# Kernel tuning notes

Hardware: AMD Instinct MI355X
Metric: run time of the kernel (lower is better)

## Reference

```python
import jax, jax.numpy as jnp
import numpy as np

B, S, D, H = 2, 2048, 1024, 16
DH = D // H          # 64, even -> RoPE valid
ROPE_BASE = 10000.0
LN_EPS = 1e-5


def _rope_cache(seq_len, head_dim, dtype):
    half = head_dim // 2
    inv_freq = 1.0 / (ROPE_BASE ** (jnp.arange(half, dtype=jnp.float32) / half))
    t = jnp.arange(seq_len, dtype=jnp.float32)
    freqs = t[:, None] * inv_freq[None, :]            # [S, half]
    emb = jnp.concatenate([freqs, freqs], axis=-1)    # [S, DH]
    return jnp.cos(emb).astype(dtype)[None, None], jnp.sin(emb).astype(dtype)[None, None]


def _rotate_every_two(x):
    x_even = x[..., ::2]
    x_odd = x[..., 1::2]
    return jnp.stack([-x_odd, x_even], axis=-1).reshape(x.shape)


def setup_inputs() -> dict:
    key = jax.random.key(0)
    ks = jax.random.split(key, 4)
    w = lambda k, shape: (jax.random.normal(k, shape, jnp.float32) * 0.02)
    return {
        "x_qk": jax.random.normal(ks[0], (B, S, D), jnp.float32),
        "x_v": jax.random.normal(ks[1], (B, S, D), jnp.float32),
        "W_qk": w(ks[2], (D, 2 * D)),
        "b_qk": jnp.zeros((2 * D,), jnp.float32),
        "W_v": w(ks[3], (D, D)),
        "b_v": jnp.zeros((D,), jnp.float32),
        "ln_gamma": jnp.ones((D,), jnp.float32),
        "ln_beta": jnp.zeros((D,), jnp.float32),
    }


def reference(x_qk, x_v, W_qk, b_qk, W_v, b_v, ln_gamma, ln_beta):
    b, s, d = x_qk.shape
    # fused QK projection -> [B,S,2,H,DH]
    qk = (x_qk @ W_qk + b_qk).reshape(b, s, 2, H, DH)
    q = jnp.transpose(qk[:, :, 0], (0, 2, 1, 3))  # [B,H,S,DH]
    k = jnp.transpose(qk[:, :, 1], (0, 2, 1, 3))
    v = jnp.transpose((x_v @ W_v + b_v).reshape(b, s, H, DH), (0, 2, 1, 3))

    cos, sin = _rope_cache(s, DH, q.dtype)
    q = q * cos + _rotate_every_two(q) * sin
    k = k * cos + _rotate_every_two(k) * sin

    scale = 1.0 / jnp.sqrt(jnp.asarray(DH, q.dtype))
    scores = jnp.einsum("bhqd,bhkd->bhqk", q, k) * scale
    probs = jax.nn.softmax(scores, axis=-1)
    attn = jnp.einsum("bhqk,bhkd->bhqd", probs, v)      # [B,H,S,DH]
    attn = jnp.transpose(attn, (0, 2, 1, 3)).reshape(b, s, d)

    mu = jnp.mean(attn, axis=-1, keepdims=True)
    var = jnp.var(attn, axis=-1, keepdims=True)
    out = (attn - mu) * jax.lax.rsqrt(var + LN_EPS) * ln_gamma + ln_beta
    return out
```

## Files before the change

kernel.cpp:

```cpp
#include <hip/hip_runtime.h>
#include <hip/hip_bf16.h>

#define Bn 2
#define Sn 2048
#define Dn 1024
#define Hn 16
#define DHn 64
#define Kd 1024
#define Mn (Bn * Sn)
#define LN10K 9.210340371976184f

typedef __attribute__((ext_vector_type(8))) short bf16x8;
typedef __attribute__((ext_vector_type(4))) float f32x4;
typedef __attribute__((ext_vector_type(16))) float f32x16;

static __device__ __forceinline__ ushort f2bf(float f) {
    uint u = __float_as_uint(f);
    u += 0x7fff + ((u >> 16) & 1);
    return (ushort)(u >> 16);
}
static __device__ __forceinline__ uint cvtpk(float a, float b) {
    uint r;
    asm("v_cvt_pk_bf16_f32 %0, %1, %2" : "=v"(r) : "v"(a), "v"(b));
    return r;
}
static __device__ __forceinline__ void plswap(uint& a, uint& b) {
    asm volatile("v_permlane32_swap_b32 %0, %1" : "+v"(a), "+v"(b));
}

#define MFMA16(a, b, c) __builtin_amdgcn_mfma_f32_16x16x32_bf16((a), (b), (c), 0, 0, 0)
#define MFMA32(a, b, c) __builtin_amdgcn_mfma_f32_32x32x16_bf16((a), (b), (c), 0, 0, 0)

static __device__ __forceinline__ void gload16(const ushort* g, ushort* l) {
    __builtin_amdgcn_global_load_lds(
        (const __attribute__((address_space(1))) void*)g,
        (__attribute__((address_space(3))) void*)l, 16, 0, 0);
}

static __device__ __forceinline__ int swz(int row, int col16) {
    return row * 128 + (((col16) * 16) ^ ((row & 7) << 4));
}

__global__ __launch_bounds__(256) void rope_tab(float* __restrict__ ct,
                                                float* __restrict__ st)
{
    const int idx = blockIdx.x * 256 + threadIdx.x;
    const int s = idx >> 5, fe = idx & 31;
    const float f = expf(-LN10K * (float)fe / 32.0f);
    const float a = (float)s * f;
    ct[idx] = cosf(a);
    st[idx] = sinf(a);
}

__global__ __launch_bounds__(256) void cvt_bf16(const float* __restrict__ in,
                                                ushort* __restrict__ out)
{
    const size_t i = ((size_t)blockIdx.x * 256 + threadIdx.x) * 8;
    const float4 a = *(const float4*)(in + i);
    const float4 b = *(const float4*)(in + i + 4);
    ushort4 lo = make_ushort4(f2bf(a.x), f2bf(a.y), f2bf(a.z), f2bf(a.w));
    ushort4 hi = make_ushort4(f2bf(b.x), f2bf(b.y), f2bf(b.z), f2bf(b.w));
    *(ushort4*)(out + i) = lo;
    *(ushort4*)(out + i + 4) = hi;
}

__global__ __launch_bounds__(256) void transpose_bf16(
    const float* __restrict__ in, ushort* __restrict__ out, int R, int C)
{
    __shared__ ushort t[32][33];
    const int n0 = blockIdx.x * 32, k0 = blockIdx.y * 32;
    const int x = threadIdx.x, y = threadIdx.y;
#pragma unroll
    for (int i = 0; i < 4; ++i)
        t[y + 8 * i][x] = f2bf(in[(size_t)(k0 + y + 8 * i) * C + n0 + x]);
    __syncthreads();
#pragma unroll
    for (int i = 0; i < 4; ++i)
        out[(size_t)(n0 + y + 8 * i) * R + k0 + x] = t[x][y + 8 * i];
}

template <int MODE>
__global__ __launch_bounds__(256) void gemm_mfma(
    const ushort* __restrict__ A, const ushort* __restrict__ Bt,
    const float* __restrict__ bias, const float* __restrict__ ctab,
    const float* __restrict__ stab, ushort* __restrict__ o0,
    ushort* __restrict__ o1)
{
    __shared__ ushort Asm[128 * 64];
    __shared__ ushort Bsm[128 * 64];

    const int tid = threadIdx.x;
    const int lane = tid & 63, w = tid >> 6;
    const int g = lane >> 4, c = lane & 15;
    const int mbase = blockIdx.y * 128;
    const int nbase = blockIdx.x * 128;
    const int wm = (w >> 1) * 64, wn = (w & 1) * 64;

    f32x4 acc[4][4];
#pragma unroll
    for (int mf = 0; mf < 4; ++mf)
#pragma unroll
        for (int nf = 0; nf < 4; ++nf)
            acc[mf][nf] = (f32x4){0.f, 0.f, 0.f, 0.f};

    const int sbase = w * 64 + lane;

    for (int k0 = 0; k0 < Kd; k0 += 64) {
#pragma unroll
        for (int j = 0; j < 4; ++j) {
            const int i = j * 256 + sbase;
            const int row = i >> 3, c16 = i & 7;
            const int kc = (c16 ^ (row & 7)) * 8;
            gload16(A + (size_t)(mbase + row) * Kd + k0 + kc,
                    &Asm[(size_t)(j * 256 + w * 64) * 8]);
            gload16(Bt + (size_t)(nbase + row) * Kd + k0 + kc,
                    &Bsm[(size_t)(j * 256 + w * 64) * 8]);
        }
        __syncthreads();

#pragma unroll
        for (int ks = 0; ks < 2; ++ks) {
            bf16x8 af[4], bfr[4];
#pragma unroll
            for (int mf = 0; mf < 4; ++mf) {
                const int row = wm + mf * 16 + c;
                af[mf] = *(const bf16x8*)((const char*)Asm + swz(row, ks * 4 + g));
            }
#pragma unroll
            for (int nf = 0; nf < 4; ++nf) {
                const int row = wn + nf * 16 + c;
                bfr[nf] = *(const bf16x8*)((const char*)Bsm + swz(row, ks * 4 + g));
            }
#pragma unroll
            for (int mf = 0; mf < 4; ++mf)
#pragma unroll
                for (int nf = 0; nf < 4; ++nf)
                    acc[mf][nf] = MFMA16(af[mf], bfr[nf], acc[mf][nf]);
        }
        __syncthreads();
    }

#pragma unroll
    for (int nf = 0; nf < 4; ++nf) {
        const int col = nbase + wn + nf * 16 + c;
        const float bs = bias[col];
        if (MODE == 0) {
            const int dh = col & 63, h = (col >> 6) & 15, isK = col >> 10;
            ushort* dst = isK ? o1 : o0;
            const float sc = isK ? 1.0f : 0.18033688011112042f;
            const float* cr = ctab + (dh & 31);
            const float* sr = stab + (dh & 31);
#pragma unroll
            for (int mf = 0; mf < 4; ++mf) {
#pragma unroll
                for (int r = 0; r < 4; ++r) {
                    const int row = mbase + wm + mf * 16 + g * 4 + r;
                    const int s = row & 2047, b = row >> 11;
                    const float v = acc[mf][nf][r] + bs;
                    const float p = __shfl_xor(v, 1);
                    const float cs = cr[s * 32], sn = sr[s * 32];
                    const float ov = (c & 1) ? v * cs + p * sn
                                             : v * cs - p * sn;
                    dst[(((size_t)(b * Hn + h)) * Sn + s) * DHn + dh] =
                        f2bf(ov * sc);
                }
            }
        } else {
            const int h = col >> 6, dh = col & 63;
#pragma unroll
            for (int mf = 0; mf < 4; ++mf) {
#pragma unroll
                for (int r = 0; r < 4; ++r) {
                    const int row = mbase + wm + mf * 16 + g * 4 + r;
                    const int s = row & 2047, b = row >> 11;
                    const float v = acc[mf][nf][r] + bs;
                    o0[(((size_t)(b * Hn + h)) * DHn + dh) * Sn + s] = f2bf(v);
                }
            }
        }
    }
}

__global__ __launch_bounds__(256) void attn_mfma(
    const ushort* __restrict__ Qg, const ushort* __restrict__ Kg,
    const ushort* __restrict__ Vtg, float* __restrict__ Aw)
{
    __shared__ char Kt[3][8192];
    __shared__ char Vt[3][8192];

    const int tid = threadIdx.x;
    const int lane = tid & 63, w = tid >> 6;
    const int r31 = lane & 31, hi = lane >> 5;
    const int bh = blockIdx.y;
    const int b = bh >> 4, h = bh & 15;
    const int q0 = blockIdx.x * 128 + w * 32;

    const ushort* qp = Qg + ((size_t)bh * Sn + q0 + r31) * DHn + hi * 8;
    bf16x8 qf[4];
#pragma unroll
    for (int kt = 0; kt < 4; ++kt)
        qf[kt] = *(const bf16x8*)(qp + kt * 16);

    const ushort* Kb = Kg + (size_t)bh * Sn * DHn;
    const ushort* Vb = Vtg + (size_t)bh * DHn * Sn;

    auto stage = [&](int buf, int kb) {
#pragma unroll
        for (int j = 0; j < 2; ++j) {
            const int i = j * 256 + w * 64 + lane;
            const int row = i >> 3, c16 = i & 7;
            const int kc = (c16 ^ (row & 7)) * 8;
            gload16(Kb + (size_t)(kb + row) * DHn + kc,
                    (ushort*)&Kt[buf][(j * 256 + w * 64) * 16]);
            gload16(Vb + (size_t)row * Sn + kb + kc,
                    (ushort*)&Vt[buf][(j * 256 + w * 64) * 16]);
        }
    };

    stage(0, 0);
    stage(1, 64);

    f32x16 acc0, acc1;
#pragma unroll
    for (int i = 0; i < 16; ++i) { acc0[i] = 0.f; acc1[i] = 0.f; }
    float m = -1e30f, lp = 0.f;

    const int NT = Sn / 64;
    for (int t = 0; t < NT; ++t) {
        const int cur = t % 3;

        if (t < NT - 1) {
            asm volatile("s_waitcnt vmcnt(4)" ::: "memory");
        } else {
            asm volatile("s_waitcnt vmcnt(0)" ::: "memory");
        }
        __builtin_amdgcn_sched_barrier(0);
        __builtin_amdgcn_s_barrier();
        __builtin_amdgcn_sched_barrier(0);

        f32x16 C0, C1;
#pragma unroll
        for (int i = 0; i < 16; ++i) { C0[i] = 0.f; C1[i] = 0.f; }
        __builtin_amdgcn_s_setprio(1);
#pragma unroll
        for (int kt = 0; kt < 4; ++kt) {
            const bf16x8 ka = *(const bf16x8*)&Kt[cur][swz(r31, kt * 2 + hi)];
            C0 = MFMA32(ka, qf[kt], C0);
        }
#pragma unroll
        for (int kt = 0; kt < 4; ++kt) {
            const bf16x8 ka = *(const bf16x8*)&Kt[cur][swz(32 + r31, kt * 2 + hi)];
            C1 = MFMA32(ka, qf[kt], C1);
        }
        __builtin_amdgcn_s_setprio(0);

        float mx[8];
#pragma unroll
        for (int i = 0; i < 8; ++i)
            mx[i] = fmaxf(fmaxf(C0[i], C0[i + 8]), fmaxf(C1[i], C1[i + 8]));
        mx[0] = fmaxf(mx[0], mx[4]); mx[1] = fmaxf(mx[1], mx[5]);
        mx[2] = fmaxf(mx[2], mx[6]); mx[3] = fmaxf(mx[3], mx[7]);
        float pmax = fmaxf(fmaxf(mx[0], mx[1]), fmaxf(mx[2], mx[3]));
        pmax = fmaxf(pmax, __shfl_xor(pmax, 32));

        if (__any(pmax > m + 11.5f)) {
            const float mn = fmaxf(m, pmax);
            const float a = exp2f(m - mn);
            m = mn;
            lp *= a;
#pragma unroll
            for (int reg = 0; reg < 16; ++reg) {
                const int qr = (reg & 3) + 8 * (reg >> 2) + 4 * hi;
                const float ar = __shfl(a, qr);
                acc0[reg] *= ar;
                acc1[reg] *= ar;
            }
        }

        bf16x8 paf[4];
#pragma unroll
        for (int tile = 0; tile < 2; ++tile) {
            const f32x16& C = tile ? C1 : C0;
            float e[16];
#pragma unroll
            for (int i = 0; i < 16; ++i) e[i] = exp2f(C[i] - m);
            float s = 0.f;
#pragma unroll
            for (int i = 0; i < 16; ++i) s += e[i];
            lp += s;
            uint p01 = cvtpk(e[0], e[1]),  p23 = cvtpk(e[2], e[3]);
            uint p45 = cvtpk(e[4], e[5]),  p67 = cvtpk(e[6], e[7]);
            uint p89 = cvtpk(e[8], e[9]),  pab = cvtpk(e[10], e[11]);
            uint pcd = cvtpk(e[12], e[13]), pef = cvtpk(e[14], e[15]);
            plswap(p01, p45); plswap(p23, p67);
            plswap(p89, pcd); plswap(pab, pef);
            uint4 f0 = {p01, p23, p45, p67};
            uint4 f1 = {p89, pab, pcd, pef};
            paf[tile * 2 + 0] = *(const bf16x8*)&f0;
            paf[tile * 2 + 1] = *(const bf16x8*)&f1;
        }

        __builtin_amdgcn_s_setprio(1);
#pragma unroll
        for (int kf = 0; kf < 4; ++kf) {
            const bf16x8 v0 = *(const bf16x8*)&Vt[cur][swz(r31, kf * 2 + hi)];
            acc0 = MFMA32(paf[kf], v0, acc0);
        }
#pragma unroll
        for (int kf = 0; kf < 4; ++kf) {
            const bf16x8 v1 = *(const bf16x8*)&Vt[cur][swz(32 + r31, kf * 2 + hi)];
            acc1 = MFMA32(paf[kf], v1, acc1);
        }
        __builtin_amdgcn_s_setprio(0);

        __builtin_amdgcn_sched_barrier(0);
        if (t + 2 < NT) stage((t + 2) % 3, (t + 2) * 64);
    }

    const float lv = lp + __shfl_xor(lp, 32);
    const float inv = 1.0f / lv;
#pragma unroll
    for (int reg = 0; reg < 16; ++reg) {
        const int qr = (reg & 3) + 8 * (reg >> 2) + 4 * hi;
        const float ir = __shfl(inv, qr);
        const int qs = q0 + qr;
        float* dst = &Aw[((size_t)b * Sn + qs) * Dn + h * DHn + r31];
        dst[0]  = acc0[reg] * ir;
        dst[32] = acc1[reg] * ir;
    }
}

__global__ __launch_bounds__(256) void ln_kernel(
    const float* __restrict__ Aw, const float* __restrict__ gamma,
    const float* __restrict__ beta, float* __restrict__ out)
{
    const int row = blockIdx.x;
    const int tid = threadIdx.x;
    const int d0 = tid * 4;
    const float4 x = *(const float4*)&Aw[(size_t)row * Dn + d0];
    float sum = x.x + x.y + x.z + x.w;
    float sq = x.x * x.x + x.y * x.y + x.z * x.z + x.w * x.w;
    for (int off = 32; off; off >>= 1) {
        sum += __shfl_xor(sum, off);
        sq += __shfl_xor(sq, off);
    }
    __shared__ float red[8];
    const int lane = tid & 63, wave = tid >> 6;
    if (lane == 0) { red[wave] = sum; red[wave + 4] = sq; }
    __syncthreads();
    if (tid == 0) {
        red[0] = red[0] + red[1] + red[2] + red[3];
        red[4] = red[4] + red[5] + red[6] + red[7];
    }
    __syncthreads();
    sum = red[0]; sq = red[4];
    const float mu = sum * (1.0f / Dn);
    const float var = sq * (1.0f / Dn) - mu * mu;
    const float rs = rsqrtf(var + 1e-5f);

    const float4 gv = *(const float4*)&gamma[d0];
    const float4 bv = *(const float4*)&beta[d0];
    float4 ov;
    ov.x = (x.x - mu) * rs * gv.x + bv.x;
    ov.y = (x.y - mu) * rs * gv.y + bv.y;
    ov.z = (x.z - mu) * rs * gv.z + bv.z;
    ov.w = (x.w - mu) * rs * gv.w + bv.w;
    *(float4*)&out[(size_t)row * Dn + d0] = ov;
}

extern "C" void kernel_launch(void* const* d_in, const int* in_sizes, int n_in,
                              void* d_out, int out_size, void* d_ws, size_t ws_size,
                              hipStream_t stream)
{
    const float* x_qk = (const float*)d_in[0];
    const float* x_v  = (const float*)d_in[1];
    const float* W_qk = (const float*)d_in[2];
    const float* b_qk = (const float*)d_in[3];
    const float* W_v  = (const float*)d_in[4];
    const float* b_v  = (const float*)d_in[5];
    const float* g    = (const float*)d_in[6];
    const float* be   = (const float*)d_in[7];

    char* ws = (char*)d_ws;
    ushort* Qw    = (ushort*)(ws);
    ushort* Kw    = (ushort*)(ws + (8u  << 20));
    ushort* Vtw   = (ushort*)(ws + (16u << 20));
    float*  Aw    = (float*) (ws + (24u << 20));
    ushort* xqkB  = (ushort*)(ws + (40u << 20));
    ushort* xvB   = (ushort*)(ws + (48u << 20));
    ushort* WqkT  = (ushort*)(ws + (56u << 20));
    ushort* WvT   = (ushort*)(ws + (60u << 20));
    float*  ctab  = (float*) (ws + (62u << 20));
    float*  stab  = (float*) (ws + (62u << 20) + (256u << 10));

    rope_tab<<<256, 256, 0, stream>>>(ctab, stab);
    cvt_bf16<<<2048, 256, 0, stream>>>(x_qk, xqkB);
    cvt_bf16<<<2048, 256, 0, stream>>>(x_v, xvB);
    transpose_bf16<<<dim3(64, 32), dim3(32, 8), 0, stream>>>(W_qk, WqkT, Kd, 2048);
    transpose_bf16<<<dim3(32, 32), dim3(32, 8), 0, stream>>>(W_v, WvT, Kd, 1024);

    gemm_mfma<0><<<dim3(16, 32), 256, 0, stream>>>(
        xqkB, WqkT, b_qk, ctab, stab, Qw, Kw);
    gemm_mfma<1><<<dim3(8, 32), 256, 0, stream>>>(
        xvB, WvT, b_v, ctab, stab, Vtw, nullptr);

    attn_mfma<<<dim3(16, 32), 256, 0, stream>>>(Qw, Kw, Vtw, Aw);
    ln_kernel<<<Bn * Sn, 256, 0, stream>>>(Aw, g, be, (float*)d_out);
}
```

Baseline: 168.3 us.

## Merge preprocessing kernels into one launch and fuse QK and V projection GEMMs

Combines rope table generation, input bf16 conversion and weight transposes into a single block-indexed prep kernel. The QK and V projection GEMMs are merged into one launch whose grid covers both, choosing inputs and epilogue per block. This removes several kernel launches and inter-kernel gaps and improves wave occupancy across the GPU, at the cost of a runtime branch in the epilogue and divergent block roles.

```diff
diff --git a/kernel.cpp b/kernel.cpp
--- a/kernel.cpp
+++ b/kernel.cpp
@@ -41,59 +41,74 @@
     return row * 128 + (((col16) * 16) ^ ((row & 7) << 4));
 }
 
-__global__ __launch_bounds__(256) void rope_tab(float* __restrict__ ct,
-                                                float* __restrict__ st)
+__global__ __launch_bounds__(256) void prep(
+    const float* __restrict__ x_qk, const float* __restrict__ x_v,
+    const float* __restrict__ W_qk, const float* __restrict__ W_v,
+    ushort* __restrict__ xqkB, ushort* __restrict__ xvB,
+    ushort* __restrict__ WqkT, ushort* __restrict__ WvT,
+    float* __restrict__ ct, float* __restrict__ st)
 {
-    const int idx = blockIdx.x * 256 + threadIdx.x;
-    const int s = idx >> 5, fe = idx & 31;
-    const float f = expf(-LN10K * (float)fe / 32.0f);
-    const float a = (float)s * f;
-    ct[idx] = cosf(a);
-    st[idx] = sinf(a);
-}
-
-__global__ __launch_bounds__(256) void cvt_bf16(const float* __restrict__ in,
-                                                ushort* __restrict__ out)
-{
-    const size_t i = ((size_t)blockIdx.x * 256 + threadIdx.x) * 8;
-    const float4 a = *(const float4*)(in + i);
-    const float4 b = *(const float4*)(in + i + 4);
-    ushort4 lo = make_ushort4(f2bf(a.x), f2bf(a.y), f2bf(a.z), f2bf(a.w));
-    ushort4 hi = make_ushort4(f2bf(b.x), f2bf(b.y), f2bf(b.z), f2bf(b.w));
-    *(ushort4*)(out + i) = lo;
-    *(ushort4*)(out + i + 4) = hi;
-}
-
-__global__ __launch_bounds__(256) void transpose_bf16(
-    const float* __restrict__ in, ushort* __restrict__ out, int R, int C)
-{
-    __shared__ ushort t[32][33];
-    const int n0 = blockIdx.x * 32, k0 = blockIdx.y * 32;
-    const int x = threadIdx.x, y = threadIdx.y;
-#pragma unroll
-    for (int i = 0; i < 4; ++i)
-        t[y + 8 * i][x] = f2bf(in[(size_t)(k0 + y + 8 * i) * C + n0 + x]);
-    __syncthreads();
-#pragma unroll
-    for (int i = 0; i < 4; ++i)
-        out[(size_t)(n0 + y + 8 * i) * R + k0 + x] = t[x][y + 8 * i];
-}
-
-template <int MODE>
-__global__ __launch_bounds__(256) void gemm_mfma(
-    const ushort* __restrict__ A, const ushort* __restrict__ Bt,
-    const float* __restrict__ bias, const float* __restrict__ ctab,
-    const float* __restrict__ stab, ushort* __restrict__ o0,
-    ushort* __restrict__ o1)
+    __shared__ ushort tle[32][33];
+    const int blk = blockIdx.x;
+    const int tid = threadIdx.x;
+
+    if (blk < 4096) {
+        const float* in = (blk < 2048) ? x_qk : x_v;
+        ushort* out = (blk < 2048) ? xqkB : xvB;
+        const int lb = (blk < 2048) ? blk : blk - 2048;
+        const size_t i = ((size_t)lb * 256 + tid) * 8;
+        const float4 a = *(const float4*)(in + i);
+        const float4 b = *(const float4*)(in + i + 4);
+        *(ushort4*)(out + i) =
+            make_ushort4(f2bf(a.x), f2bf(a.y), f2bf(a.z), f2bf(a.w));
+        *(ushort4*)(out + i + 4) =
+            make_ushort4(f2bf(b.x), f2bf(b.y), f2bf(b.z), f2bf(b.w));
+    } else if (blk < 7168) {
+        const bool isQK = blk < 6144;
+        const int t = isQK ? blk - 4096 : blk - 6144;
+        const int C = isQK ? 2048 : 1024;
+        const float* in = isQK ? W_qk : W_v;
+        ushort* out = isQK ? WqkT : WvT;
+        const int n0 = (isQK ? (t & 63) : (t & 31)) * 32;
+        const int k0 = (isQK ? (t >> 6) : (t >> 5)) * 32;
+        const int x = tid & 31, y = tid >> 5;
+#pragma unroll
+        for (int i = 0; i < 4; ++i)
+            tle[y + 8 * i][x] = f2bf(in[(size_t)(k0 + y + 8 * i) * C + n0 + x]);
+        __syncthreads();
+#pragma unroll
+        for (int i = 0; i < 4; ++i)
+            out[(size_t)(n0 + y + 8 * i) * Kd + k0 + x] = tle[x][y + 8 * i];
+    } else {
+        const int idx = (blk - 7168) * 256 + tid;
+        const int s = idx >> 5, fe = idx & 31;
+        const float f = expf(-LN10K * (float)fe / 32.0f);
+        const float a = (float)s * f;
+        ct[idx] = cosf(a);
+        st[idx] = sinf(a);
+    }
+}
+
+__global__ __launch_bounds__(256) void gemm_fused_all(
+    const ushort* __restrict__ xqkB, const ushort* __restrict__ xvB,
+    const ushort* __restrict__ WqkT, const ushort* __restrict__ WvT,
+    const float* __restrict__ b_qk, const float* __restrict__ b_v,
+    const float* __restrict__ ctab, const float* __restrict__ stab,
+    ushort* __restrict__ Qw, ushort* __restrict__ Kw, ushort* __restrict__ Vtw)
 {
     __shared__ ushort Asm[128 * 64];
     __shared__ ushort Bsm[128 * 64];
 
+    const bool isQK = blockIdx.x < 16;
+    const ushort* A  = isQK ? xqkB : xvB;
+    const ushort* Bt = isQK ? WqkT : WvT;
+    const float* bias = isQK ? b_qk : b_v;
+    const int nbase = (isQK ? blockIdx.x : blockIdx.x - 16) * 128;
+    const int mbase = blockIdx.y * 128;
+
     const int tid = threadIdx.x;
     const int lane = tid & 63, w = tid >> 6;
     const int g = lane >> 4, c = lane & 15;
-    const int mbase = blockIdx.y * 128;
-    const int nbase = blockIdx.x * 128;
     const int wm = (w >> 1) * 64, wn = (w & 1) * 64;
 
     f32x4 acc[4][4];
@@ -144,9 +159,9 @@
     for (int nf = 0; nf < 4; ++nf) {
         const int col = nbase + wn + nf * 16 + c;
         const float bs = bias[col];
-        if (MODE == 0) {
+        if (isQK) {
             const int dh = col & 63, h = (col >> 6) & 15, isK = col >> 10;
-            ushort* dst = isK ? o1 : o0;
+            ushort* dst = isK ? Kw : Qw;
             const float sc = isK ? 1.0f : 0.18033688011112042f;
             const float* cr = ctab + (dh & 31);
             const float* sr = stab + (dh & 31);
@@ -174,7 +189,7 @@
                     const int row = mbase + wm + mf * 16 + g * 4 + r;
                     const int s = row & 2047, b = row >> 11;
                     const float v = acc[mf][nf][r] + bs;
-                    o0[(((size_t)(b * Hn + h)) * DHn + dh) * Sn + s] = f2bf(v);
+                    Vtw[(((size_t)(b * Hn + h)) * DHn + dh) * Sn + s] = f2bf(v);
                 }
             }
         }
@@ -393,17 +408,10 @@
     float*  ctab  = (float*) (ws + (62u << 20));
     float*  stab  = (float*) (ws + (62u << 20) + (256u << 10));
 
-    rope_tab<<<256, 256, 0, stream>>>(ctab, stab);
-    cvt_bf16<<<2048, 256, 0, stream>>>(x_qk, xqkB);
-    cvt_bf16<<<2048, 256, 0, stream>>>(x_v, xvB);
-    transpose_bf16<<<dim3(64, 32), dim3(32, 8), 0, stream>>>(W_qk, WqkT, Kd, 2048);
-    transpose_bf16<<<dim3(32, 32), dim3(32, 8), 0, stream>>>(W_v, WvT, Kd, 1024);
-
-    gemm_mfma<0><<<dim3(16, 32), 256, 0, stream>>>(
-        xqkB, WqkT, b_qk, ctab, stab, Qw, Kw);
-    gemm_mfma<1><<<dim3(8, 32), 256, 0, stream>>>(
-        xvB, WvT, b_v, ctab, stab, Vtw, nullptr);
-
+    prep<<<7424, 256, 0, stream>>>(x_qk, x_v, W_qk, W_v,
+                                   xqkB, xvB, WqkT, WvT, ctab, stab);
+    gemm_fused_all<<<dim3(24, 32), 256, 0, stream>>>(
+        xqkB, xvB, WqkT, WvT, b_qk, b_v, ctab, stab, Qw, Kw, Vtw);
     attn_mfma<<<dim3(16, 32), 256, 0, stream>>>(Qw, Kw, Vtw, Aw);
     ln_kernel<<<Bn * Sn, 256, 0, stream>>>(Aw, g, be, (float*)d_out);
 }
```

Measured after the change: 137.6 us, median of 2. -18.2%, faster.
